# Kernel tuning notes

Hardware: AMD Instinct MI355X
Metric: run time of the kernel (lower is better)

The kernel has to match this reference:

```python
import jax, jax.numpy as jnp
import numpy as np

B, S, E, H, D, RD = 1, 2048, 2560, 32, 80, 32  # batch, seq, n_embd, heads, head_dim, rotary_dim


def setup_inputs() -> dict:
    key = jax.random.key(0)
    k0, k1, k2 = jax.random.split(key, 3)
    hidden_states = jax.random.normal(k0, (B, S, E), dtype=jnp.float32)
    Wqkv_w = jax.random.normal(k1, (3 * E, E), dtype=jnp.float32) * 0.02
    Wqkv_b = jnp.zeros((3 * E,), dtype=jnp.float32)
    out_w = jax.random.normal(k2, (E, E), dtype=jnp.float32) * 0.02
    out_b = jnp.zeros((E,), dtype=jnp.float32)
    # RotaryEmbedding tables: inv_freq over even indices of rotary_dim
    inv_freq = 1.0 / (10000.0 ** (jnp.arange(0, RD, 2, dtype=jnp.float32) / RD))  # [RD/2]
    t = jnp.arange(S, dtype=jnp.float32)
    freqs = t[:, None] * inv_freq[None, :]  # [S, RD/2]
    return {
        "hidden_states": hidden_states,
        "Wqkv_w": Wqkv_w,
        "Wqkv_b": Wqkv_b,
        "out_w": out_w,
        "out_b": out_b,
        "cos": jnp.cos(freqs),
        "sin": jnp.sin(freqs),
    }


def _apply_rotary(x, cos, sin):
    # x: [B, S, H, D]; rotate first 2*cos.shape[-1] dims (GPT-NeoX half-split style)
    rd = cos.shape[-1] * 2
    x_rot, x_pass = x[..., :rd], x[..., rd:]
    x1, x2 = jnp.split(x_rot, 2, axis=-1)
    c = cos[None, :, None, :]  # [1, S, 1, rd/2]
    s = sin[None, :, None, :]
    rotated = jnp.concatenate([x1 * c - x2 * s, x1 * s + x2 * c], axis=-1)
    return jnp.concatenate([rotated, x_pass], axis=-1)


def reference(hidden_states, Wqkv_w, Wqkv_b, out_w, out_b, cos, sin):
    b, s, e = hidden_states.shape
    qkv = hidden_states @ Wqkv_w.T + Wqkv_b              # [B, S, 3E]
    qkv = qkv.reshape(b, s, 3, H, D)
    q = _apply_rotary(qkv[:, :, 0], cos[:s], sin[:s])    # [B, S, H, D]
    k = _apply_rotary(qkv[:, :, 1], cos[:s], sin[:s])
    v = qkv[:, :, 2]
    scale = 1.0 / np.sqrt(D).astype(np.float32)
    scores = jnp.einsum("bthd,bshd->bhts", q, k) * scale  # [B, H, S, S]
    causal = jnp.triu(jnp.full((s, s), -10000.0, dtype=scores.dtype), 1)
    scores = scores + causal
    attn = jax.nn.softmax(scores, axis=-1)
    out = jnp.einsum("bhts,bshd->bthd", attn, v).reshape(b, s, H * D)
    return out @ out_w.T + out_b
```

## Files before the change

kernel.cpp:

```cpp
#include <hip/hip_runtime.h>
#include <hip/hip_bf16.h>

typedef __attribute__((ext_vector_type(8))) __bf16 bf16x8;
typedef __attribute__((ext_vector_type(8))) short s16x8;
typedef __attribute__((ext_vector_type(4))) float f32x4;
typedef unsigned short u16;
typedef unsigned int u32;

static __device__ __forceinline__ float bf2f(u16 u) {
  union { unsigned int i; float f; } x;
  x.i = ((unsigned int)u) << 16;
  return x.f;
}
static __device__ __forceinline__ u16 f2bf(float f) {
  __hip_bfloat16 h = __float2bfloat16(f);
  return __builtin_bit_cast(u16, h);
}

__global__ void cvt3_kernel(const float* __restrict__ s0, u16* __restrict__ d0, int n0,
                            const float* __restrict__ s1, u16* __restrict__ d1, int n1,
                            const float* __restrict__ s2, u16* __restrict__ d2, int n2) {
  const int stride = gridDim.x * blockDim.x;
  const int t0 = blockIdx.x * blockDim.x + threadIdx.x;
  for (int i = t0; i < n0; i += stride) {
    float4 f = reinterpret_cast<const float4*>(s0)[i];
    ushort4 u{f2bf(f.x), f2bf(f.y), f2bf(f.z), f2bf(f.w)};
    reinterpret_cast<ushort4*>(d0)[i] = u;
  }
  for (int i = t0; i < n1; i += stride) {
    float4 f = reinterpret_cast<const float4*>(s1)[i];
    ushort4 u{f2bf(f.x), f2bf(f.y), f2bf(f.z), f2bf(f.w)};
    reinterpret_cast<ushort4*>(d1)[i] = u;
  }
  for (int i = t0; i < n2; i += stride) {
    float4 f = reinterpret_cast<const float4*>(s2)[i];
    ushort4 u{f2bf(f.x), f2bf(f.y), f2bf(f.z), f2bf(f.w)};
    reinterpret_cast<ushort4*>(d2)[i] = u;
  }
}

template <typename OUT_T>
__global__ __launch_bounds__(512, 4) void gemm128x256_bt(
    const u16* __restrict__ A, const u16* __restrict__ B,
    const float* __restrict__ bias, OUT_T* __restrict__ C,
    int M, int N, int K) {
  __shared__ u16 As[2][128 * 32];
  __shared__ u16 Bs[2][256 * 32];
  const int tid = threadIdx.x;
  const int w = tid >> 6;
  const int lane = tid & 63;
  const int g = lane >> 4, c = lane & 15;
  const int wm = w >> 2, wn = w & 3;
  const int nwg = gridDim.x * gridDim.y;
  const int flat = blockIdx.y * gridDim.x + blockIdx.x;
  const int swz = (flat & 7) * (nwg >> 3) + (flat >> 3);
  const int bx = swz % gridDim.x, by = swz / gridDim.x;
  const int row0 = by * 128, col0 = bx * 256;
  const int nt = K >> 5;

  f32x4 acc[4][4] = {};

  auto issueA = [&](int t, u16* lds) {
    int q = tid;
    int r = q >> 2;
    int cl = (q & 3) ^ ((r >> 1) & 3);
    const u16* gp = A + (size_t)(row0 + r) * K + (t << 5) + cl * 8;
    __builtin_amdgcn_global_load_lds(
        (const __attribute__((address_space(1))) void*)gp,
        (__attribute__((address_space(3))) void*)(lds + q * 8), 16, 0, 0);
  };
  auto issueB = [&](int t, u16* lds) {
#pragma unroll
    for (int rr = 0; rr < 2; ++rr) {
      int q = rr * 512 + tid;
      int r = q >> 2;
      int cl = (q & 3) ^ ((r >> 1) & 3);
      const u16* gp = B + (size_t)(col0 + r) * K + (t << 5) + cl * 8;
      __builtin_amdgcn_global_load_lds(
          (const __attribute__((address_space(1))) void*)gp,
          (__attribute__((address_space(3))) void*)(lds + q * 8), 16, 0, 0);
    }
  };

  issueA(0, As[0]);
  issueB(0, Bs[0]);

  int cur = 0;
  for (int t = 0; t < nt; ++t) {
    if (t + 1 < nt) {
      issueA(t + 1, As[cur ^ 1]);
      issueB(t + 1, Bs[cur ^ 1]);
      asm volatile("s_waitcnt vmcnt(3)" ::: "memory");
    } else {
      asm volatile("s_waitcnt vmcnt(0)" ::: "memory");
    }
    __builtin_amdgcn_s_barrier();

    bf16x8 afr[4], bfr[4];
#pragma unroll
    for (int mi = 0; mi < 4; ++mi) {
      int rowa = wm * 64 + mi * 16 + c;
      int p = g ^ ((rowa >> 1) & 3);
      afr[mi] = *reinterpret_cast<const bf16x8*>(&As[cur][(rowa * 4 + p) * 8]);
    }
#pragma unroll
    for (int ni = 0; ni < 4; ++ni) {
      int rowb = wn * 64 + ni * 16 + c;
      int p = g ^ ((rowb >> 1) & 3);
      bfr[ni] = *reinterpret_cast<const bf16x8*>(&Bs[cur][(rowb * 4 + p) * 8]);
    }
    __builtin_amdgcn_s_setprio(1);
#pragma unroll
    for (int mi = 0; mi < 4; ++mi)
#pragma unroll
      for (int ni = 0; ni < 4; ++ni)
        acc[mi][ni] = __builtin_amdgcn_mfma_f32_16x16x32_bf16(
            afr[mi], bfr[ni], acc[mi][ni], 0, 0, 0);
    __builtin_amdgcn_s_setprio(0);
    __builtin_amdgcn_s_barrier();
    cur ^= 1;
  }

#pragma unroll
  for (int mi = 0; mi < 4; ++mi) {
#pragma unroll
    for (int ni = 0; ni < 4; ++ni) {
      int col = col0 + wn * 64 + ni * 16 + c;
      float bs = bias[col];
#pragma unroll
      for (int r = 0; r < 4; ++r) {
        int row = row0 + wm * 64 + mi * 16 + g * 4 + r;
        float v = acc[mi][ni][r] + bs;
        if constexpr (sizeof(OUT_T) == 2) {
          C[(size_t)row * N + col] = f2bf(v);
        } else {
          C[(size_t)row * N + col] = v;
        }
      }
    }
  }
}

template <typename OUT_T>
__global__ __launch_bounds__(256, 2) void gemm128p_bt(
    const u16* __restrict__ A, const u16* __restrict__ B,
    const float* __restrict__ bias, OUT_T* __restrict__ C,
    int M, int N, int K) {
  __shared__ u16 As[2][128 * 64];
  __shared__ u16 Bs[2][128 * 64];
  const int tid = threadIdx.x;
  const int w = tid >> 6;
  const int lane = tid & 63;
  const int g = lane >> 4, c = lane & 15;
  const int wm = w >> 1, wn = w & 1;
  const int nwg = gridDim.x * gridDim.y;
  const int flat = blockIdx.y * gridDim.x + blockIdx.x;
  const int swz = (flat & 7) * (nwg >> 3) + (flat >> 3);
  const int bx = swz % gridDim.x, by = swz / gridDim.x;
  const int row0 = by * 128, col0 = bx * 128;
  const int nt = K >> 6;

  f32x4 acc[4][4] = {};

  auto issue = [&](const u16* __restrict__ base, int rb, int t, u16* lds) {
#pragma unroll
    for (int rr = 0; rr < 4; ++rr) {
      int q = rr * 256 + tid;
      int r = q >> 3;
      int cl = (q & 7) ^ (r & 7);
      const u16* gp = base + (size_t)(rb + r) * K + (t << 6) + cl * 8;
      __builtin_amdgcn_global_load_lds(
          (const __attribute__((address_space(1))) void*)gp,
          (__attribute__((address_space(3))) void*)(lds + q * 8), 16, 0, 0);
    }
  };

  issue(A, row0, 0, As[0]);
  issue(B, col0, 0, Bs[0]);

  int cur = 0;
  for (int t = 0; t < nt; ++t) {
    if (t + 1 < nt) {
      issue(A, row0, t + 1, As[cur ^ 1]);
      issue(B, col0, t + 1, Bs[cur ^ 1]);
      asm volatile("s_waitcnt vmcnt(8)" ::: "memory");
    } else {
      asm volatile("s_waitcnt vmcnt(0)" ::: "memory");
    }
    __builtin_amdgcn_s_barrier();

#pragma unroll
    for (int kk = 0; kk < 2; ++kk) {
      bf16x8 afr[4], bfr[4];
      const int p = (kk * 4 + g) ^ (c & 7);
#pragma unroll
      for (int mi = 0; mi < 4; ++mi) {
        int rowa = wm * 64 + mi * 16 + c;
        afr[mi] = *reinterpret_cast<const bf16x8*>(&As[cur][(rowa * 8 + p) * 8]);
      }
#pragma unroll
      for (int ni = 0; ni < 4; ++ni) {
        int rowb = wn * 64 + ni * 16 + c;
        bfr[ni] = *reinterpret_cast<const bf16x8*>(&Bs[cur][(rowb * 8 + p) * 8]);
      }
      __builtin_amdgcn_s_setprio(1);
#pragma unroll
      for (int mi = 0; mi < 4; ++mi)
#pragma unroll
        for (int ni = 0; ni < 4; ++ni)
          acc[mi][ni] = __builtin_amdgcn_mfma_f32_16x16x32_bf16(
              afr[mi], bfr[ni], acc[mi][ni], 0, 0, 0);
      __builtin_amdgcn_s_setprio(0);
      __builtin_amdgcn_s_barrier();
    }
    cur ^= 1;
  }

#pragma unroll
  for (int mi = 0; mi < 4; ++mi) {
#pragma unroll
    for (int ni = 0; ni < 4; ++ni) {
      int col = col0 + wn * 64 + ni * 16 + c;
      float bs = bias[col];
#pragma unroll
      for (int r = 0; r < 4; ++r) {
        int row = row0 + wm * 64 + mi * 16 + g * 4 + r;
        float v = acc[mi][ni][r] + bs;
        if constexpr (sizeof(OUT_T) == 2) {
          C[(size_t)row * N + col] = f2bf(v);
        } else {
          C[(size_t)row * N + col] = v;
        }
      }
    }
  }
}

__global__ __launch_bounds__(256) void ropev_kernel(
    const u16* __restrict__ qkv, const float* __restrict__ cosT,
    const float* __restrict__ sinT, u16* __restrict__ Qp, u16* __restrict__ Kp,
    u16* __restrict__ Vt) {
  __shared__ u16 Vs[80 * 136];
  const int h = blockIdx.y;
  const int tid = threadIdx.x;
  const int d = tid & 127;
  const int sh = tid >> 7;
  const float scale = 0.16129822f;
#pragma unroll
  for (int i = 0; i < 8; ++i) {
    const int s = blockIdx.x * 16 + i * 2 + sh;
    const size_t row = (size_t)s * 7680;
    if (d < 96) {
      float qo = 0.f, ko = 0.f;
      if (d < 80) {
        float q = bf2f(qkv[row + h * 80 + d]);
        float k = bf2f(qkv[row + 2560 + h * 80 + d]);
        if (d < 16) {
          float cs = cosT[s * 16 + d], sn = sinT[s * 16 + d];
          float q2 = bf2f(qkv[row + h * 80 + d + 16]);
          float k2 = bf2f(qkv[row + 2560 + h * 80 + d + 16]);
          qo = q * cs - q2 * sn;
          ko = k * cs - k2 * sn;
        } else if (d < 32) {
          float cs = cosT[s * 16 + d - 16], sn = sinT[s * 16 + d - 16];
          float q1 = bf2f(qkv[row + h * 80 + d - 16]);
          float k1 = bf2f(qkv[row + 2560 + h * 80 + d - 16]);
          qo = q1 * sn + q * cs;
          ko = k1 * sn + k * cs;
        } else {
          qo = q;
          ko = k;
        }
      }
      size_t o = ((size_t)h * 2048 + s) * 96 + d;
      Qp[o] = f2bf(qo * scale);
      Kp[o] = f2bf(ko);
    }
  }

  const int u = blockIdx.y * gridDim.x + blockIdx.x;
  if (u < 512) {
    const int s0 = (u & 15) * 128;
    const int hv = u >> 4;
    const int s = tid >> 1;
    const int h2 = tid & 1;
#pragma unroll
    for (int j = 0; j < 5; ++j) {
      s16x8 v = *reinterpret_cast<const s16x8*>(
          &qkv[(size_t)(s0 + s) * 7680 + 5120 + hv * 80 + h2 * 40 + j * 8]);
#pragma unroll
      for (int e = 0; e < 8; ++e)
        Vs[(h2 * 40 + j * 8 + e) * 136 + s] = (u16)v[e];
    }
    __syncthreads();
    for (int idx = tid; idx < 80 * 16; idx += 256) {
      int dd = idx >> 4, s8 = idx & 15;
      s16x8 v = *reinterpret_cast<const s16x8*>(&Vs[dd * 136 + s8 * 8]);
      *reinterpret_cast<s16x8*>(&Vt[((size_t)(hv * 80 + dd)) * 2048 + s0 + s8 * 8]) = v;
    }
  }
}

__global__ __launch_bounds__(256, 2) void attn_kernel(
    const u16* __restrict__ Qp, const u16* __restrict__ Kp,
    const u16* __restrict__ Vt, u16* __restrict__ O) {
  __shared__ u32 Plds[4][32 * 36];
  __shared__ float mbuf[4][2][16];
  const int tid = threadIdx.x;
  const int w = tid >> 6;
  const int lane = tid & 63;
  const int g = lane >> 4, c = lane & 15;
  const int f = blockIdx.x;
  const int xcd = f & 7;
  const int k_ = f >> 3;
  const int h = (xcd << 2) | (k_ & 3);
  const int qb = 63 - (k_ >> 2);
  const int q0 = qb * 32;
  const size_t hq = (size_t)h * 2048;
  u32* Pw = &Plds[w][0];

  bf16x8 bq[2][3];
#pragma unroll
  for (int qi = 0; qi < 2; ++qi)
#pragma unroll
    for (int ch = 0; ch < 3; ++ch)
      bq[qi][ch] = *reinterpret_cast<const bf16x8*>(
          &Qp[(hq + q0 + qi * 16 + c) * 96 + ch * 32 + g * 8]);

  f32x4 accO[2][5] = {};
  float mrow[2] = {-1e30f, -1e30f};
  float lrow[2] = {0.f, 0.f};

  const int nkb = (q0 + 95) >> 6;
  for (int kbi = w; kbi < nkb; kbi += 4) {
    const int kb = kbi << 6;
    bf16x8 ak[4][3];
#pragma unroll
    for (int ki = 0; ki < 4; ++ki)
#pragma unroll
      for (int ch = 0; ch < 3; ++ch)
        ak[ki][ch] = *reinterpret_cast<const bf16x8*>(
            &Kp[(hq + kb + ki * 16 + c) * 96 + ch * 32 + g * 8]);
    bf16x8 av[5][2];
#pragma unroll
    for (int db = 0; db < 5; ++db)
#pragma unroll
      for (int kc = 0; kc < 2; ++kc)
        av[db][kc] = *reinterpret_cast<const bf16x8*>(
            &Vt[((size_t)h * 80 + db * 16 + c) * 2048 + kb + kc * 32 + g * 8]);

    f32x4 SS[4][2] = {};
    __builtin_amdgcn_s_setprio(1);
#pragma unroll
    for (int ch = 0; ch < 3; ++ch)
#pragma unroll
      for (int ki = 0; ki < 4; ++ki)
#pragma unroll
        for (int qi = 0; qi < 2; ++qi)
          SS[ki][qi] = __builtin_amdgcn_mfma_f32_16x16x32_bf16(
              ak[ki][ch], bq[qi][ch], SS[ki][qi], 0, 0, 0);
    __builtin_amdgcn_s_setprio(0);

    if (kbi == nkb - 1) {
#pragma unroll
      for (int ki = 0; ki < 4; ++ki)
#pragma unroll
        for (int qi = 0; qi < 2; ++qi)
#pragma unroll
          for (int r = 0; r < 4; ++r) {
            int k = kb + ki * 16 + g * 4 + r;
            int q = q0 + qi * 16 + c;
            if (k > q) SS[ki][qi][r] -= 14426.95f;
          }
    }

    float pmax[2];
    bool need = false;
#pragma unroll
    for (int qi = 0; qi < 2; ++qi) {
      float m2 = SS[0][qi][0];
#pragma unroll
      for (int ki = 0; ki < 4; ++ki)
#pragma unroll
        for (int r = 0; r < 4; ++r)
          if (ki | r) m2 = fmaxf(m2, SS[ki][qi][r]);
      m2 = fmaxf(m2, __shfl_xor(m2, 16));
      m2 = fmaxf(m2, __shfl_xor(m2, 32));
      pmax[qi] = m2;
      need = need || (m2 > mrow[qi] + 8.0f);
    }
    if (__any(need)) {
#pragma unroll
      for (int qi = 0; qi < 2; ++qi) {
        float mnew = fmaxf(mrow[qi], pmax[qi]);
        float sc = __builtin_amdgcn_exp2f(mrow[qi] - mnew);
        lrow[qi] *= sc;
#pragma unroll
        for (int db = 0; db < 5; ++db) accO[qi][db] *= sc;
        mrow[qi] = mnew;
      }
    }
#pragma unroll
    for (int qi = 0; qi < 2; ++qi) {
      float rs = 0.f;
#pragma unroll
      for (int ki = 0; ki < 4; ++ki)
#pragma unroll
        for (int r = 0; r < 4; ++r) {
          float pv = __builtin_amdgcn_exp2f(SS[ki][qi][r] - mrow[qi]);
          SS[ki][qi][r] = pv;
          rs += pv;
        }
      rs += __shfl_xor(rs, 16);
      rs += __shfl_xor(rs, 32);
      lrow[qi] += rs;
    }

#pragma unroll
    for (int qi = 0; qi < 2; ++qi)
#pragma unroll
      for (int ki = 0; ki < 4; ++ki)
#pragma unroll
        for (int r2 = 0; r2 < 2; ++r2) {
          u32 lo = f2bf(SS[ki][qi][r2 * 2]);
          u32 hi = f2bf(SS[ki][qi][r2 * 2 + 1]);
          Pw[(qi * 16 + c) * 36 + ki * 8 + g * 2 + r2] = lo | (hi << 16);
        }
    bf16x8 pa[2][2];
#pragma unroll
    for (int qi = 0; qi < 2; ++qi)
#pragma unroll
      for (int kc = 0; kc < 2; ++kc)
        pa[qi][kc] = *reinterpret_cast<const bf16x8*>(
            &Pw[(qi * 16 + c) * 36 + kc * 16 + g * 4]);

    __builtin_amdgcn_s_setprio(1);
#pragma unroll
    for (int kc = 0; kc < 2; ++kc)
#pragma unroll
      for (int db = 0; db < 5; ++db)
#pragma unroll
        for (int qi = 0; qi < 2; ++qi)
          accO[qi][db] = __builtin_amdgcn_mfma_f32_16x16x32_bf16(
              av[db][kc], pa[qi][kc], accO[qi][db], 0, 0, 0);
    __builtin_amdgcn_s_setprio(0);
  }

  mbuf[w][0][c] = mrow[0];
  mbuf[w][1][c] = mrow[1];
  __syncthreads();
#pragma unroll
  for (int qi = 0; qi < 2; ++qi) {
    float ms = fmaxf(fmaxf(mbuf[0][qi][c], mbuf[1][qi][c]),
                     fmaxf(mbuf[2][qi][c], mbuf[3][qi][c]));
    float fl = __builtin_amdgcn_exp2f(mrow[qi] - ms);
    lrow[qi] *= fl;
#pragma unroll
    for (int db = 0; db < 5; ++db) accO[qi][db] *= fl;
  }
  float* mg = (float*)&Plds[0][0] + lane * 44;
  if (w == 0) {
#pragma unroll
    for (int qi = 0; qi < 2; ++qi)
#pragma unroll
      for (int db = 0; db < 5; ++db)
        *reinterpret_cast<f32x4*>(mg + (qi * 5 + db) * 4) = accO[qi][db];
    mg[40] = lrow[0];
    mg[41] = lrow[1];
  }
  __syncthreads();
  if (w == 1) {
#pragma unroll
    for (int qi = 0; qi < 2; ++qi)
#pragma unroll
      for (int db = 0; db < 5; ++db) {
        f32x4 t = *reinterpret_cast<f32x4*>(mg + (qi * 5 + db) * 4);
        *reinterpret_cast<f32x4*>(mg + (qi * 5 + db) * 4) = t + accO[qi][db];
      }
    mg[40] += lrow[0];
    mg[41] += lrow[1];
  }
  __syncthreads();
  if (w == 2) {
#pragma unroll
    for (int qi = 0; qi < 2; ++qi)
#pragma unroll
      for (int db = 0; db < 5; ++db) {
        f32x4 t = *reinterpret_cast<f32x4*>(mg + (qi * 5 + db) * 4);
        *reinterpret_cast<f32x4*>(mg + (qi * 5 + db) * 4) = t + accO[qi][db];
      }
    mg[40] += lrow[0];
    mg[41] += lrow[1];
  }
  __syncthreads();
  if (w == 3) {
    float lf[2];
    lf[0] = 1.0f / (mg[40] + lrow[0]);
    lf[1] = 1.0f / (mg[41] + lrow[1]);
#pragma unroll
    for (int qi = 0; qi < 2; ++qi)
#pragma unroll
      for (int db = 0; db < 5; ++db) {
        f32x4 t = *reinterpret_cast<f32x4*>(mg + (qi * 5 + db) * 4);
        t = t + accO[qi][db];
        ushort4 o4;
        o4.x = f2bf(t[0] * lf[qi]);
        o4.y = f2bf(t[1] * lf[qi]);
        o4.z = f2bf(t[2] * lf[qi]);
        o4.w = f2bf(t[3] * lf[qi]);
        *reinterpret_cast<ushort4*>(
            &O[(size_t)(q0 + qi * 16 + c) * 2560 + h * 80 + db * 16 + g * 4]) = o4;
      }
  }
}

extern "C" void kernel_launch(void* const* d_in, const int* in_sizes, int n_in,
                              void* d_out, int out_size, void* d_ws, size_t ws_size,
                              hipStream_t stream) {
  const float* hs = (const float*)d_in[0];
  const float* Wqkv_w = (const float*)d_in[1];
  const float* Wqkv_b = (const float*)d_in[2];
  const float* out_w = (const float*)d_in[3];
  const float* out_b = (const float*)d_in[4];
  const float* cosT = (const float*)d_in[5];
  const float* sinT = (const float*)d_in[6];
  float* out = (float*)d_out;

  u16* ws = (u16*)d_ws;
  u16* hsb = ws;
  u16* wqkvb = hsb + (size_t)2048 * 2560;
  u16* outwb = wqkvb + (size_t)7680 * 2560;
  u16* qkv = outwb + (size_t)2560 * 2560;
  u16* Qp = qkv + (size_t)2048 * 7680;
  u16* Kp = Qp + (size_t)32 * 2048 * 96;
  u16* Vt = Kp + (size_t)32 * 2048 * 96;
  u16* attn = qkv;

  cvt3_kernel<<<dim3(2048), dim3(256), 0, stream>>>(
      hs, hsb, 5242880 / 4, Wqkv_w, wqkvb, 19660800 / 4, out_w, outwb, 6553600 / 4);

  gemm128x256_bt<u16><<<dim3(30, 16), dim3(512), 0, stream>>>(
      hsb, wqkvb, Wqkv_b, qkv, 2048, 7680, 2560);
  ropev_kernel<<<dim3(128, 32), dim3(256), 0, stream>>>(qkv, cosT, sinT, Qp, Kp, Vt);
  attn_kernel<<<dim3(2048), dim3(256), 0, stream>>>(Qp, Kp, Vt, attn);
  gemm128p_bt<float><<<dim3(20, 16), dim3(256), 0, stream>>>(attn, outwb, out_b, out,
                                                             2048, 2560, 2560);
}
```

Measured before the change: 256.9 us.

## Double attention query tile to 64 rows per block, reusing K/V loads

Each attention block now handles 64 query rows instead of 32, splitting the score computation into two 32-row halves that share the same K and V fragments, and the grid is halved. This amortizes the K/V global loads over twice as many queries. The cost is more registers for accumulators and Q fragments, larger LDS, fewer blocks for load balancing, and some wasted masked work on the diagonal tile.

Measured after the change: 244.7 us, median of 2. -4.8%, faster.

```diff
diff --git a/kernel.cpp b/kernel.cpp
--- a/kernel.cpp
+++ b/kernel.cpp
@@ -304,8 +304,8 @@
 __global__ __launch_bounds__(256, 2) void attn_kernel(
     const u16* __restrict__ Qp, const u16* __restrict__ Kp,
     const u16* __restrict__ Vt, u16* __restrict__ O) {
-  __shared__ u32 Plds[4][32 * 36];
-  __shared__ float mbuf[4][2][16];
+  __shared__ u32 Plds[4][64 * 36];
+  __shared__ float mbuf[4][4][16];
   const int tid = threadIdx.x;
   const int w = tid >> 6;
   const int lane = tid & 63;
@@ -314,24 +314,24 @@
   const int xcd = f & 7;
   const int k_ = f >> 3;
   const int h = (xcd << 2) | (k_ & 3);
-  const int qb = 63 - (k_ >> 2);
-  const int q0 = qb * 32;
+  const int pb = 31 - (k_ >> 2);
+  const int q0 = pb * 64;
   const size_t hq = (size_t)h * 2048;
   u32* Pw = &Plds[w][0];
 
-  bf16x8 bq[2][3];
-#pragma unroll
-  for (int qi = 0; qi < 2; ++qi)
+  bf16x8 bq[4][3];
+#pragma unroll
+  for (int qi = 0; qi < 4; ++qi)
 #pragma unroll
     for (int ch = 0; ch < 3; ++ch)
       bq[qi][ch] = *reinterpret_cast<const bf16x8*>(
           &Qp[(hq + q0 + qi * 16 + c) * 96 + ch * 32 + g * 8]);
 
-  f32x4 accO[2][5] = {};
-  float mrow[2] = {-1e30f, -1e30f};
-  float lrow[2] = {0.f, 0.f};
-
-  const int nkb = (q0 + 95) >> 6;
+  f32x4 accO[4][5] = {};
+  float mrow[4] = {-1e30f, -1e30f, -1e30f, -1e30f};
+  float lrow[4] = {0.f, 0.f, 0.f, 0.f};
+
+  const int nkb = pb + 1;
   for (int kbi = w; kbi < nkb; kbi += 4) {
     const int kb = kbi << 6;
     bf16x8 ak[4][3];
@@ -341,6 +341,90 @@
       for (int ch = 0; ch < 3; ++ch)
         ak[ki][ch] = *reinterpret_cast<const bf16x8*>(
             &Kp[(hq + kb + ki * 16 + c) * 96 + ch * 32 + g * 8]);
+
+#pragma unroll
+    for (int qh = 0; qh < 2; ++qh) {
+      f32x4 SS[4][2] = {};
+      __builtin_amdgcn_s_setprio(1);
+#pragma unroll
+      for (int ch = 0; ch < 3; ++ch)
+#pragma unroll
+        for (int ki = 0; ki < 4; ++ki)
+#pragma unroll
+          for (int j = 0; j < 2; ++j)
+            SS[ki][j] = __builtin_amdgcn_mfma_f32_16x16x32_bf16(
+                ak[ki][ch], bq[qh * 2 + j][ch], SS[ki][j], 0, 0, 0);
+      __builtin_amdgcn_s_setprio(0);
+
+      if (kbi == nkb - 1) {
+#pragma unroll
+        for (int ki = 0; ki < 4; ++ki)
+#pragma unroll
+          for (int j = 0; j < 2; ++j)
+#pragma unroll
+            for (int r = 0; r < 4; ++r) {
+              int k = kb + ki * 16 + g * 4 + r;
+              int q = q0 + (qh * 2 + j) * 16 + c;
+              if (k > q) SS[ki][j][r] -= 14426.95f;
+            }
+      }
+
+      float pmax[2];
+      bool need = false;
+#pragma unroll
+      for (int j = 0; j < 2; ++j) {
+        float m2 = SS[0][j][0];
+#pragma unroll
+        for (int ki = 0; ki < 4; ++ki)
+#pragma unroll
+          for (int r = 0; r < 4; ++r)
+            if (ki | r) m2 = fmaxf(m2, SS[ki][j][r]);
+        m2 = fmaxf(m2, __shfl_xor(m2, 16));
+        m2 = fmaxf(m2, __shfl_xor(m2, 32));
+        pmax[j] = m2;
+        need = need || (m2 > mrow[qh * 2 + j] + 8.0f);
+      }
+      if (__any(need)) {
+#pragma unroll
+        for (int j = 0; j < 2; ++j) {
+          int qi = qh * 2 + j;
+          float mnew = fmaxf(mrow[qi], pmax[j]);
+          float sc = __builtin_amdgcn_exp2f(mrow[qi] - mnew);
+          lrow[qi] *= sc;
+#pragma unroll
+          for (int db = 0; db < 5; ++db) accO[qi][db] *= sc;
+          mrow[qi] = mnew;
+        }
+      }
+#pragma unroll
+      for (int j = 0; j < 2; ++j) {
+        int qi = qh * 2 + j;
+        float rs = 0.f;
+#pragma unroll
+        for (int ki = 0; ki < 4; ++ki)
+#pragma unroll
+          for (int r = 0; r < 4; ++r) {
+            float pv = __builtin_amdgcn_exp2f(SS[ki][j][r] - mrow[qi]);
+            SS[ki][j][r] = pv;
+            rs += pv;
+          }
+        rs += __shfl_xor(rs, 16);
+        rs += __shfl_xor(rs, 32);
+        lrow[qi] += rs;
+      }
+#pragma unroll
+      for (int j = 0; j < 2; ++j)
+#pragma unroll
+        for (int ki = 0; ki < 4; ++ki)
+#pragma unroll
+          for (int r2 = 0; r2 < 2; ++r2) {
+            u32 lo = f2bf(SS[ki][j][r2 * 2]);
+            u32 hi = f2bf(SS[ki][j][r2 * 2 + 1]);
+            Pw[((qh * 2 + j) * 16 + c) * 36 + ki * 8 + g * 2 + r2] =
+                lo | (hi << 16);
+          }
+    }
+
     bf16x8 av[5][2];
 #pragma unroll
     for (int db = 0; db < 5; ++db)
@@ -349,108 +433,29 @@
         av[db][kc] = *reinterpret_cast<const bf16x8*>(
             &Vt[((size_t)h * 80 + db * 16 + c) * 2048 + kb + kc * 32 + g * 8]);
 
-    f32x4 SS[4][2] = {};
     __builtin_amdgcn_s_setprio(1);
 #pragma unroll
-    for (int ch = 0; ch < 3; ++ch)
-#pragma unroll
-      for (int ki = 0; ki < 4; ++ki)
-#pragma unroll
-        for (int qi = 0; qi < 2; ++qi)
-          SS[ki][qi] = __builtin_amdgcn_mfma_f32_16x16x32_bf16(
-              ak[ki][ch], bq[qi][ch], SS[ki][qi], 0, 0, 0);
+    for (int qi = 0; qi < 4; ++qi) {
+      bf16x8 pa[2];
+#pragma unroll
+      for (int kc = 0; kc < 2; ++kc)
+        pa[kc] = *reinterpret_cast<const bf16x8*>(
+            &Pw[(qi * 16 + c) * 36 + kc * 16 + g * 4]);
+#pragma unroll
+      for (int kc = 0; kc < 2; ++kc)
+#pragma unroll
+        for (int db = 0; db < 5; ++db)
+          accO[qi][db] = __builtin_amdgcn_mfma_f32_16x16x32_bf16(
+              av[db][kc], pa[kc], accO[qi][db], 0, 0, 0);
+    }
     __builtin_amdgcn_s_setprio(0);
-
-    if (kbi == nkb - 1) {
-#pragma unroll
-      for (int ki = 0; ki < 4; ++ki)
-#pragma unroll
-        for (int qi = 0; qi < 2; ++qi)
-#pragma unroll
-          for (int r = 0; r < 4; ++r) {
-            int k = kb + ki * 16 + g * 4 + r;
-            int q = q0 + qi * 16 + c;
-            if (k > q) SS[ki][qi][r] -= 14426.95f;
-          }
-    }
-
-    float pmax[2];
-    bool need = false;
-#pragma unroll
-    for (int qi = 0; qi < 2; ++qi) {
-      float m2 = SS[0][qi][0];
-#pragma unroll
-      for (int ki = 0; ki < 4; ++ki)
-#pragma unroll
-        for (int r = 0; r < 4; ++r)
-          if (ki | r) m2 = fmaxf(m2, SS[ki][qi][r]);
-      m2 = fmaxf(m2, __shfl_xor(m2, 16));
-      m2 = fmaxf(m2, __shfl_xor(m2, 32));
-      pmax[qi] = m2;
-      need = need || (m2 > mrow[qi] + 8.0f);
-    }
-    if (__any(need)) {
-#pragma unroll
-      for (int qi = 0; qi < 2; ++qi) {
-        float mnew = fmaxf(mrow[qi], pmax[qi]);
-        float sc = __builtin_amdgcn_exp2f(mrow[qi] - mnew);
-        lrow[qi] *= sc;
-#pragma unroll
-        for (int db = 0; db < 5; ++db) accO[qi][db] *= sc;
-        mrow[qi] = mnew;
-      }
-    }
-#pragma unroll
-    for (int qi = 0; qi < 2; ++qi) {
-      float rs = 0.f;
-#pragma unroll
-      for (int ki = 0; ki < 4; ++ki)
-#pragma unroll
-        for (int r = 0; r < 4; ++r) {
-          float pv = __builtin_amdgcn_exp2f(SS[ki][qi][r] - mrow[qi]);
-          SS[ki][qi][r] = pv;
-          rs += pv;
-        }
-      rs += __shfl_xor(rs, 16);
-      rs += __shfl_xor(rs, 32);
-      lrow[qi] += rs;
-    }
-
-#pragma unroll
-    for (int qi = 0; qi < 2; ++qi)
-#pragma unroll
-      for (int ki = 0; ki < 4; ++ki)
-#pragma unroll
-        for (int r2 = 0; r2 < 2; ++r2) {
-          u32 lo = f2bf(SS[ki][qi][r2 * 2]);
-          u32 hi = f2bf(SS[ki][qi][r2 * 2 + 1]);
-          Pw[(qi * 16 + c) * 36 + ki * 8 + g * 2 + r2] = lo | (hi << 16);
-        }
-    bf16x8 pa[2][2];
-#pragma unroll
-    for (int qi = 0; qi < 2; ++qi)
-#pragma unroll
-      for (int kc = 0; kc < 2; ++kc)
-        pa[qi][kc] = *reinterpret_cast<const bf16x8*>(
-            &Pw[(qi * 16 + c) * 36 + kc * 16 + g * 4]);
-
-    __builtin_amdgcn_s_setprio(1);
-#pragma unroll
-    for (int kc = 0; kc < 2; ++kc)
-#pragma unroll
-      for (int db = 0; db < 5; ++db)
-#pragma unroll
-        for (int qi = 0; qi < 2; ++qi)
-          accO[qi][db] = __builtin_amdgcn_mfma_f32_16x16x32_bf16(
-              av[db][kc], pa[qi][kc], accO[qi][db], 0, 0, 0);
-    __builtin_amdgcn_s_setprio(0);
-  }
-
-  mbuf[w][0][c] = mrow[0];
-  mbuf[w][1][c] = mrow[1];
+  }
+
+#pragma unroll
+  for (int qi = 0; qi < 4; ++qi) mbuf[w][qi][c] = mrow[qi];
   __syncthreads();
 #pragma unroll
-  for (int qi = 0; qi < 2; ++qi) {
+  for (int qi = 0; qi < 4; ++qi) {
     float ms = fmaxf(fmaxf(mbuf[0][qi][c], mbuf[1][qi][c]),
                      fmaxf(mbuf[2][qi][c], mbuf[3][qi][c]));
     float fl = __builtin_amdgcn_exp2f(mrow[qi] - ms);
@@ -458,59 +463,58 @@
 #pragma unroll
     for (int db = 0; db < 5; ++db) accO[qi][db] *= fl;
   }
-  float* mg = (float*)&Plds[0][0] + lane * 44;
+  float* mg = (float*)&Plds[0][0] + lane * 84;
   if (w == 0) {
 #pragma unroll
-    for (int qi = 0; qi < 2; ++qi)
+    for (int qi = 0; qi < 4; ++qi)
 #pragma unroll
       for (int db = 0; db < 5; ++db)
         *reinterpret_cast<f32x4*>(mg + (qi * 5 + db) * 4) = accO[qi][db];
-    mg[40] = lrow[0];
-    mg[41] = lrow[1];
+#pragma unroll
+    for (int qi = 0; qi < 4; ++qi) mg[80 + qi] = lrow[qi];
   }
   __syncthreads();
   if (w == 1) {
 #pragma unroll
-    for (int qi = 0; qi < 2; ++qi)
+    for (int qi = 0; qi < 4; ++qi)
 #pragma unroll
       for (int db = 0; db < 5; ++db) {
         f32x4 t = *reinterpret_cast<f32x4*>(mg + (qi * 5 + db) * 4);
         *reinterpret_cast<f32x4*>(mg + (qi * 5 + db) * 4) = t + accO[qi][db];
       }
-    mg[40] += lrow[0];
-    mg[41] += lrow[1];
+#pragma unroll
+    for (int qi = 0; qi < 4; ++qi) mg[80 + qi] += lrow[qi];
   }
   __syncthreads();
   if (w == 2) {
 #pragma unroll
-    for (int qi = 0; qi < 2; ++qi)
+    for (int qi = 0; qi < 4; ++qi)
 #pragma unroll
       for (int db = 0; db < 5; ++db) {
         f32x4 t = *reinterpret_cast<f32x4*>(mg + (qi * 5 + db) * 4);
         *reinterpret_cast<f32x4*>(mg + (qi * 5 + db) * 4) = t + accO[qi][db];
       }
-    mg[40] += lrow[0];
-    mg[41] += lrow[1];
+#pragma unroll
+    for (int qi = 0; qi < 4; ++qi) mg[80 + qi] += lrow[qi];
   }
   __syncthreads();
   if (w == 3) {
-    float lf[2];
-    lf[0] = 1.0f / (mg[40] + lrow[0]);
-    lf[1] = 1.0f / (mg[41] + lrow[1]);
-#pragma unroll
-    for (int qi = 0; qi < 2; ++qi)
+#pragma unroll
+    for (int qi = 0; qi < 4; ++qi) {
+      float lf = 1.0f / (mg[80 + qi] + lrow[qi]);
 #pragma unroll
       for (int db = 0; db < 5; ++db) {
         f32x4 t = *reinterpret_cast<f32x4*>(mg + (qi * 5 + db) * 4);
         t = t + accO[qi][db];
         ushort4 o4;
-        o4.x = f2bf(t[0] * lf[qi]);
-        o4.y = f2bf(t[1] * lf[qi]);
-        o4.z = f2bf(t[2] * lf[qi]);
-        o4.w = f2bf(t[3] * lf[qi]);
+        o4.x = f2bf(t[0] * lf);
+        o4.y = f2bf(t[1] * lf);
+        o4.z = f2bf(t[2] * lf);
+        o4.w = f2bf(t[3] * lf);
         *reinterpret_cast<ushort4*>(
             &O[(size_t)(q0 + qi * 16 + c) * 2560 + h * 80 + db * 16 + g * 4]) = o4;
       }
+    }
   }
 }
 
@@ -542,7 +546,7 @@
   gemm128x256_bt<u16><<<dim3(30, 16), dim3(512), 0, stream>>>(
       hsb, wqkvb, Wqkv_b, qkv, 2048, 7680, 2560);
   ropev_kernel<<<dim3(128, 32), dim3(256), 0, stream>>>(qkv, cosT, sinT, Qp, Kp, Vt);
-  attn_kernel<<<dim3(2048), dim3(256), 0, stream>>>(Qp, Kp, Vt, attn);
+  attn_kernel<<<dim3(1024), dim3(256), 0, stream>>>(Qp, Kp, Vt, attn);
   gemm128p_bt<float><<<dim3(20, 16), dim3(256), 0, stream>>>(attn, outwb, out_b, out,
                                                              2048, 2560, 2560);
 }
```
